# Optimization experiments

Measured on AMD Instinct MI355X. Metric: run time of the kernel, lower is better.

The kernel has to match this reference:

```python
import jax, jax.numpy as jnp
import numpy as np

N = 100000
F = 512
D = 128
E = 1600000

def setup_inputs() -> dict:
    key = jax.random.key(0)
    k1, k2, k3, k4, k5 = jax.random.split(key, 5)
    feature = jax.random.normal(k1, (N, F), dtype=jnp.float32)
    W = jax.random.normal(k2, (F, D), dtype=jnp.float32) * (1.0 / np.sqrt(D))
    bias = jax.random.normal(k3, (D,), dtype=jnp.float32) * (1.0 / np.sqrt(D))
    edge_vals = jax.random.uniform(k4, (E,), dtype=jnp.float32)
    edge_index = jax.random.randint(k5, (2, E), 0, N, dtype=jnp.int32)
    return {"feature": feature, "W": W, "bias": bias,
            "edge_vals": edge_vals, "edge_index": edge_index}

def reference(feature, W, bias, edge_vals, edge_index):
    # support = relu(feature @ W)                          [N, D]
    support = jax.nn.relu(feature @ W)
    row, col = edge_index[0], edge_index[1]
    # spmm(adj, support): gather source rows, scale, scatter-add to dest rows
    msgs = edge_vals[:, None] * support[col]               # [E, D]
    agg = jax.ops.segment_sum(msgs, row, num_segments=feature.shape[0])
    # adj_low = adj + I  ->  identity contributes +support; then + bias
    return agg + support + bias
```

## Files before the change

### kernel.cpp

```cpp
#include <hip/hip_runtime.h>
#include <hip/hip_bf16.h>

typedef __attribute__((ext_vector_type(8))) __bf16 bf16x8;
typedef __attribute__((ext_vector_type(4))) float f32x4;

#define F_DIM 512
#define D_DIM 128
#define RPB 128
#define MAXBUK 1024
#define BIN_CHUNK 8192

__device__ __forceinline__ unsigned short f32_to_bf16_rn(float x) {
    union { float f; unsigned u; } v; v.f = x;
    unsigned u = v.u;
    unsigned rounded = u + 0x7fffu + ((u >> 16) & 1u);
    return (unsigned short)(rounded >> 16);
}
__device__ __forceinline__ float bf16_to_f32(unsigned short u) {
    return __uint_as_float((unsigned)u << 16);
}

__global__ void wt_kernel(const float* __restrict__ W, unsigned short* __restrict__ Wt) {
    int idx = blockIdx.x * blockDim.x + threadIdx.x;
    int n = idx >> 9;
    int k = idx & 511;
    Wt[idx] = f32_to_bf16_rn(W[k * D_DIM + n]);
}

__global__ __launch_bounds__(256) void gemm_relu_pipe(
    const float* __restrict__ A,
    const unsigned short* __restrict__ Bt,
    unsigned short* __restrict__ Sb,
    int Nrows)
{
    __shared__ unsigned short Al[2 * 64 * 40];
    __shared__ unsigned short Bl[2 * 128 * 40];

    const int tid  = threadIdx.x;
    const int wave = tid >> 6;
    const int lane = tid & 63;
    const int g    = lane >> 4;
    const int r16  = lane & 15;
    const int m0   = blockIdx.x * 64;

    const int sar = tid >> 2;
    const int skq = tid & 3;
    int arow = m0 + sar;
    if (arow >= Nrows) arow = Nrows - 1;
    const float* aptr = A + (size_t)arow * F_DIM + skq * 8;
    const int awoff = sar * 40 + skq * 8;

    const int sbr = tid >> 1;
    const int skh = tid & 1;
    const unsigned short* bptr = Bt + (size_t)sbr * F_DIM + skh * 16;
    const int bwoff = sbr * 40 + skh * 16;

    float4 ar0, ar1;
    uint4  br0, br1;

    auto loadAB = [&](int ks) {
        const float4* pa = (const float4*)(aptr + ks * 32);
        ar0 = pa[0]; ar1 = pa[1];
        const uint4* pb = (const uint4*)(bptr + ks * 32);
        br0 = pb[0]; br1 = pb[1];
    };
    auto storeAB = [&](int buf) {
        union { uint4 q; __bf16 h[8]; } u;
        u.h[0]=(__bf16)ar0.x; u.h[1]=(__bf16)ar0.y; u.h[2]=(__bf16)ar0.z; u.h[3]=(__bf16)ar0.w;
        u.h[4]=(__bf16)ar1.x; u.h[5]=(__bf16)ar1.y; u.h[6]=(__bf16)ar1.z; u.h[7]=(__bf16)ar1.w;
        *(uint4*)&Al[buf * 2560 + awoff] = u.q;
        unsigned short* bw = &Bl[buf * 5120 + bwoff];
        *(uint4*)bw       = br0;
        *(uint4*)(bw + 8) = br1;
    };

    f32x4 acc[8];
#pragma unroll
    for (int j = 0; j < 8; ++j) acc[j] = (f32x4)0.0f;

    loadAB(0);
    storeAB(0);
    __syncthreads();

#pragma unroll
    for (int ks = 0; ks < 16; ++ks) {
        const int cur = ks & 1;
        if (ks < 15) loadAB(ks + 1);

        const unsigned short* Ab = Al + cur * 2560;
        const unsigned short* Bb = Bl + cur * 5120;
        bf16x8 af = *(const bf16x8*)&Ab[(wave * 16 + r16) * 40 + g * 8];
#pragma unroll
        for (int nf = 0; nf < 8; ++nf) {
            bf16x8 bf = *(const bf16x8*)&Bb[(nf * 16 + r16) * 40 + g * 8];
            acc[nf] = __builtin_amdgcn_mfma_f32_16x16x32_bf16(af, bf, acc[nf], 0, 0, 0);
        }

        if (ks < 15) storeAB(cur ^ 1);
        __syncthreads();
    }

#pragma unroll
    for (int nf = 0; nf < 8; ++nf) {
#pragma unroll
        for (int r = 0; r < 4; ++r) {
            int row = m0 + wave * 16 + g * 4 + r;
            if (row < Nrows) {
                float v = acc[nf][r];
                Sb[(size_t)row * D_DIM + nf * 16 + r16] = f32_to_bf16_rn(v > 0.f ? v : 0.f);
            }
        }
    }
}

__global__ void cursor_init_kernel(int* __restrict__ cursor, int nbuk, int cap) {
    int i = blockIdx.x * blockDim.x + threadIdx.x;
    if (i < nbuk) cursor[i] = i * cap;
}

__global__ __launch_bounds__(256) void bin_kernel(
    const int* __restrict__ ei, const float* __restrict__ ev,
    int* __restrict__ cursor, uint2* __restrict__ ecv, int E, int nbuk)
{
    __shared__ int cnt[MAXBUK];
    __shared__ int bas[MAXBUK];
    const int tid = threadIdx.x;
    const int e0 = blockIdx.x * BIN_CHUNK;
    const int e1 = min(e0 + BIN_CHUNK, E);

    for (int i = tid; i < nbuk; i += 256) cnt[i] = 0;
    __syncthreads();
    for (int e = e0 + tid; e < e1; e += 256)
        atomicAdd(&cnt[ei[e] >> 7], 1);
    __syncthreads();
    for (int i = tid; i < nbuk; i += 256) {
        int c = cnt[i];
        bas[i] = c ? atomicAdd(&cursor[i], c) : 0;
        cnt[i] = 0;
    }
    __syncthreads();
    for (int e = e0 + tid; e < e1; e += 256) {
        int r = ei[e];
        int b = r >> 7;
        int slot = atomicAdd(&cnt[b], 1);
        uint2 cv;
        cv.x = ((unsigned)ei[E + e] << 7) | (unsigned)(r & 127);
        cv.y = __float_as_uint(ev[e]);
        ecv[(size_t)bas[b] + slot] = cv;
    }
}

__global__ __launch_bounds__(256) void bsort_kernel(
    const uint2* __restrict__ ecv, const int* __restrict__ cursor,
    uint2* __restrict__ ecv2, int* __restrict__ rowoff, int* __restrict__ rowcnt,
    int cap, int Nrows)
{
    __shared__ int cnt[RPB];
    __shared__ int base[RPB];
    const int tid = threadIdx.x;
    const int b   = blockIdx.x;
    const int beg = b * cap;
    const int end = cursor[b];

    if (tid < RPB) cnt[tid] = 0;
    __syncthreads();
    for (int i = beg + tid; i < end; i += 256)
        atomicAdd(&cnt[ecv[i].x & 127], 1);
    __syncthreads();
    if (tid < 64) {
        int carry = 0;
#pragma unroll
        for (int c = 0; c < 2; ++c) {
            int idx = c * 64 + tid;
            int v = cnt[idx];
            int orig = v;
            for (int d = 1; d < 64; d <<= 1) {
                int t = __shfl_up(v, d, 64);
                if (tid >= d) v += t;
            }
            base[idx] = carry + v - orig;
            carry += __shfl(v, 63, 64);
        }
    }
    __syncthreads();
    if (tid < RPB) {
        int r = b * RPB + tid;
        if (r < Nrows) {
            rowoff[r] = beg + base[tid];
            rowcnt[r] = cnt[tid];
        }
        cnt[tid] = 0;
    }
    __syncthreads();
    for (int i = beg + tid; i < end; i += 256) {
        uint2 cv = ecv[i];
        int rl = cv.x & 127;
        int slot = atomicAdd(&cnt[rl], 1);
        ecv2[(size_t)beg + base[rl] + slot] = cv;
    }
}

__global__ __launch_bounds__(256) void accum_kernel(
    const uint2* __restrict__ ecv2, const int* __restrict__ rowoff,
    const int* __restrict__ rowcnt, const unsigned short* __restrict__ Sb,
    const float* __restrict__ bias, float* __restrict__ out, int n)
{
    int wid = (blockIdx.x * 256 + threadIdx.x) >> 6;
    if (wid >= n) return;
    int lane = threadIdx.x & 63;
    int c2 = lane * 2;

    int start = rowoff[wid];
    int end   = start + rowcnt[wid];

    float ax = 0.f, ay = 0.f;
    int i = start;
    for (; i + 3 < end; i += 4) {
        uint2 cv0 = ecv2[i];
        uint2 cv1 = ecv2[i + 1];
        uint2 cv2 = ecv2[i + 2];
        uint2 cv3 = ecv2[i + 3];
        ushort2 s0 = *(const ushort2*)&Sb[(size_t)(cv0.x >> 7) * D_DIM + c2];
        ushort2 s1 = *(const ushort2*)&Sb[(size_t)(cv1.x >> 7) * D_DIM + c2];
        ushort2 s2 = *(const ushort2*)&Sb[(size_t)(cv2.x >> 7) * D_DIM + c2];
        ushort2 s3 = *(const ushort2*)&Sb[(size_t)(cv3.x >> 7) * D_DIM + c2];
        float v0 = __uint_as_float(cv0.y);
        float v1 = __uint_as_float(cv1.y);
        float v2 = __uint_as_float(cv2.y);
        float v3 = __uint_as_float(cv3.y);
        ax += v0 * bf16_to_f32(s0.x) + v1 * bf16_to_f32(s1.x)
            + v2 * bf16_to_f32(s2.x) + v3 * bf16_to_f32(s3.x);
        ay += v0 * bf16_to_f32(s0.y) + v1 * bf16_to_f32(s1.y)
            + v2 * bf16_to_f32(s2.y) + v3 * bf16_to_f32(s3.y);
    }
    for (; i < end; ++i) {
        uint2 cv = ecv2[i];
        ushort2 s = *(const ushort2*)&Sb[(size_t)(cv.x >> 7) * D_DIM + c2];
        float v = __uint_as_float(cv.y);
        ax += v * bf16_to_f32(s.x);
        ay += v * bf16_to_f32(s.y);
    }

    ushort2 so = *(const ushort2*)&Sb[(size_t)wid * D_DIM + c2];
    float2 b = *(const float2*)&bias[c2];
    float2 o;
    o.x = ax + bf16_to_f32(so.x) + b.x;
    o.y = ay + bf16_to_f32(so.y) + b.y;
    *(float2*)&out[(size_t)wid * D_DIM + c2] = o;
}

extern "C" void kernel_launch(void* const* d_in, const int* in_sizes, int n_in,
                              void* d_out, int out_size, void* d_ws, size_t ws_size,
                              hipStream_t stream) {
    const float* feature = (const float*)d_in[0];
    const float* W       = (const float*)d_in[1];
    const float* bias    = (const float*)d_in[2];
    const float* ev      = (const float*)d_in[3];
    const int*   ei      = (const int*)d_in[4];
    float* out = (float*)d_out;

    const int N = in_sizes[0] / F_DIM;
    const int E = in_sizes[3];
    const int nbuk = (N + RPB - 1) / RPB;
    int cap = (E + nbuk - 1) / nbuk;
    cap = cap + cap / 4 + 256;

    char* ws = (char*)d_ws;
    size_t cur = 0;
    auto alloc = [&](size_t bytes) -> void* {
        void* p = ws + cur;
        cur = (cur + bytes + 255) & ~(size_t)255;
        return p;
    };
    unsigned short* Sb     = (unsigned short*)alloc((size_t)N * D_DIM * 2);
    unsigned short* Wt     = (unsigned short*)alloc((size_t)D_DIM * F_DIM * 2);
    int*            cursor = (int*)alloc((size_t)nbuk * 4);
    int*            rowoff = (int*)alloc((size_t)N * 4);
    int*            rowcnt = (int*)alloc((size_t)N * 4);
    uint2*          ecv    = (uint2*)alloc(((size_t)nbuk * cap + BIN_CHUNK) * 8);
    uint2*          ecv2   = (uint2*)alloc(((size_t)nbuk * cap + BIN_CHUNK) * 8);
    (void)ws_size;

    wt_kernel<<<(F_DIM * D_DIM) / 256, 256, 0, stream>>>(W, Wt);
    gemm_relu_pipe<<<(N + 63) / 64, 256, 0, stream>>>(feature, Wt, Sb, N);
    cursor_init_kernel<<<(nbuk + 255) / 256, 256, 0, stream>>>(cursor, nbuk, cap);
    bin_kernel<<<(E + BIN_CHUNK - 1) / BIN_CHUNK, 256, 0, stream>>>(ei, ev, cursor, ecv, E, nbuk);
    bsort_kernel<<<nbuk, 256, 0, stream>>>(ecv, cursor, ecv2, rowoff, rowcnt, cap, N);
    accum_kernel<<<(N + 3) / 4, 256, 0, stream>>>(ecv2, rowoff, rowcnt, Sb, bias, out, N);
}
```

Before: 220.1 us.

## Fuse bucket sort with row accumulation in shared memory, merge prep kernels

Bucket sorting and row aggregation now run in one kernel. Each 512-thread block loads its bucket's edges into shared memory, counting-sorts them by local row there, and then accumulates its 128 rows directly. This drops the ecv2, rowoff and rowcnt global round trips and one launch. W transposition and cursor initialisation are folded into a single prep kernel. Per-bucket capacity is clamped to 3072 entries to fit shared memory (48 KB of edge buffers). That is safe for these uniform inputs but could overflow on skewed degree distributions. Each block now covers 128 rows with 8 waves, which lowers parallelism in the gather phase.

```diff
diff --git a/kernel.cpp b/kernel.cpp
--- a/kernel.cpp
+++ b/kernel.cpp
@@ -9,6 +9,7 @@
 #define RPB 128
 #define MAXBUK 1024
 #define BIN_CHUNK 8192
+#define CAPMAX 3072
 
 __device__ __forceinline__ unsigned short f32_to_bf16_rn(float x) {
     union { float f; unsigned u; } v; v.f = x;
@@ -20,11 +21,17 @@
     return __uint_as_float((unsigned)u << 16);
 }
 
-__global__ void wt_kernel(const float* __restrict__ W, unsigned short* __restrict__ Wt) {
-    int idx = blockIdx.x * blockDim.x + threadIdx.x;
-    int n = idx >> 9;
-    int k = idx & 511;
-    Wt[idx] = f32_to_bf16_rn(W[k * D_DIM + n]);
+__global__ void prep_kernel(const float* __restrict__ W, unsigned short* __restrict__ Wt,
+                            int* __restrict__ cursor, int nbuk, int cap) {
+    int b = blockIdx.x;
+    if (b < 256) {
+        int idx = b * 256 + threadIdx.x;
+        int n = idx >> 9;
+        int k = idx & 511;
+        Wt[idx] = f32_to_bf16_rn(W[k * D_DIM + n]);
+    } else {
+        for (int i = threadIdx.x; i < nbuk; i += 256) cursor[i] = i * cap;
+    }
 }
 
 __global__ __launch_bounds__(256) void gemm_relu_pipe(
@@ -113,11 +120,6 @@
     }
 }
 
-__global__ void cursor_init_kernel(int* __restrict__ cursor, int nbuk, int cap) {
-    int i = blockIdx.x * blockDim.x + threadIdx.x;
-    if (i < nbuk) cursor[i] = i * cap;
-}
-
 __global__ __launch_bounds__(256) void bin_kernel(
     const int* __restrict__ ei, const float* __restrict__ ev,
     int* __restrict__ cursor, uint2* __restrict__ ecv, int E, int nbuk)
@@ -150,22 +152,29 @@
     }
 }
 
-__global__ __launch_bounds__(256) void bsort_kernel(
+__global__ __launch_bounds__(512) void sortaccum_kernel(
     const uint2* __restrict__ ecv, const int* __restrict__ cursor,
-    uint2* __restrict__ ecv2, int* __restrict__ rowoff, int* __restrict__ rowcnt,
-    int cap, int Nrows)
+    const unsigned short* __restrict__ Sb, const float* __restrict__ bias,
+    float* __restrict__ out, int Nrows, int cap)
 {
+    __shared__ uint2 raw[CAPMAX];
+    __shared__ uint2 srt[CAPMAX];
     __shared__ int cnt[RPB];
     __shared__ int base[RPB];
+    __shared__ int scur[RPB];
+
     const int tid = threadIdx.x;
     const int b   = blockIdx.x;
     const int beg = b * cap;
-    const int end = cursor[b];
+    const int n   = cursor[b] - beg;
 
     if (tid < RPB) cnt[tid] = 0;
     __syncthreads();
-    for (int i = beg + tid; i < end; i += 256)
-        atomicAdd(&cnt[ecv[i].x & 127], 1);
+    for (int i = tid; i < n; i += 512) {
+        uint2 cv = ecv[beg + i];
+        raw[i] = cv;
+        atomicAdd(&cnt[cv.x & 127], 1);
+    }
     __syncthreads();
     if (tid < 64) {
         int carry = 0;
@@ -178,75 +187,67 @@
                 int t = __shfl_up(v, d, 64);
                 if (tid >= d) v += t;
             }
-            base[idx] = carry + v - orig;
+            int excl = carry + v - orig;
+            base[idx] = excl;
+            scur[idx] = excl;
             carry += __shfl(v, 63, 64);
         }
     }
     __syncthreads();
-    if (tid < RPB) {
-        int r = b * RPB + tid;
-        if (r < Nrows) {
-            rowoff[r] = beg + base[tid];
-            rowcnt[r] = cnt[tid];
-        }
-        cnt[tid] = 0;
-    }
-    __syncthreads();
-    for (int i = beg + tid; i < end; i += 256) {
-        uint2 cv = ecv[i];
-        int rl = cv.x & 127;
-        int slot = atomicAdd(&cnt[rl], 1);
-        ecv2[(size_t)beg + base[rl] + slot] = cv;
-    }
-}
-
-__global__ __launch_bounds__(256) void accum_kernel(
-    const uint2* __restrict__ ecv2, const int* __restrict__ rowoff,
-    const int* __restrict__ rowcnt, const unsigned short* __restrict__ Sb,
-    const float* __restrict__ bias, float* __restrict__ out, int n)
-{
-    int wid = (blockIdx.x * 256 + threadIdx.x) >> 6;
-    if (wid >= n) return;
-    int lane = threadIdx.x & 63;
-    int c2 = lane * 2;
-
-    int start = rowoff[wid];
-    int end   = start + rowcnt[wid];
-
-    float ax = 0.f, ay = 0.f;
-    int i = start;
-    for (; i + 3 < end; i += 4) {
-        uint2 cv0 = ecv2[i];
-        uint2 cv1 = ecv2[i + 1];
-        uint2 cv2 = ecv2[i + 2];
-        uint2 cv3 = ecv2[i + 3];
-        ushort2 s0 = *(const ushort2*)&Sb[(size_t)(cv0.x >> 7) * D_DIM + c2];
-        ushort2 s1 = *(const ushort2*)&Sb[(size_t)(cv1.x >> 7) * D_DIM + c2];
-        ushort2 s2 = *(const ushort2*)&Sb[(size_t)(cv2.x >> 7) * D_DIM + c2];
-        ushort2 s3 = *(const ushort2*)&Sb[(size_t)(cv3.x >> 7) * D_DIM + c2];
-        float v0 = __uint_as_float(cv0.y);
-        float v1 = __uint_as_float(cv1.y);
-        float v2 = __uint_as_float(cv2.y);
-        float v3 = __uint_as_float(cv3.y);
-        ax += v0 * bf16_to_f32(s0.x) + v1 * bf16_to_f32(s1.x)
-            + v2 * bf16_to_f32(s2.x) + v3 * bf16_to_f32(s3.x);
-        ay += v0 * bf16_to_f32(s0.y) + v1 * bf16_to_f32(s1.y)
-            + v2 * bf16_to_f32(s2.y) + v3 * bf16_to_f32(s3.y);
-    }
-    for (; i < end; ++i) {
-        uint2 cv = ecv2[i];
-        ushort2 s = *(const ushort2*)&Sb[(size_t)(cv.x >> 7) * D_DIM + c2];
-        float v = __uint_as_float(cv.y);
-        ax += v * bf16_to_f32(s.x);
-        ay += v * bf16_to_f32(s.y);
-    }
-
-    ushort2 so = *(const ushort2*)&Sb[(size_t)wid * D_DIM + c2];
-    float2 b = *(const float2*)&bias[c2];
-    float2 o;
-    o.x = ax + bf16_to_f32(so.x) + b.x;
-    o.y = ay + bf16_to_f32(so.y) + b.y;
-    *(float2*)&out[(size_t)wid * D_DIM + c2] = o;
+    for (int i = tid; i < n; i += 512) {
+        uint2 cv = raw[i];
+        int slot = atomicAdd(&scur[cv.x & 127], 1);
+        srt[slot] = cv;
+    }
+    __syncthreads();
+
+    const int wv   = tid >> 6;
+    const int lane = tid & 63;
+    const int c2   = lane * 2;
+    const int r0g  = b * RPB;
+
+    for (int rr = 0; rr < 16; ++rr) {
+        int rl  = wv * 16 + rr;
+        int row = r0g + rl;
+        if (row >= Nrows) break;
+        int s = base[rl];
+        int e = s + cnt[rl];
+
+        float ax = 0.f, ay = 0.f;
+        int i = s;
+        for (; i + 3 < e; i += 4) {
+            uint2 cv0 = srt[i];
+            uint2 cv1 = srt[i + 1];
+            uint2 cv2 = srt[i + 2];
+            uint2 cv3 = srt[i + 3];
+            ushort2 s0 = *(const ushort2*)&Sb[(size_t)(cv0.x >> 7) * D_DIM + c2];
+            ushort2 s1 = *(const ushort2*)&Sb[(size_t)(cv1.x >> 7) * D_DIM + c2];
+            ushort2 s2 = *(const ushort2*)&Sb[(size_t)(cv2.x >> 7) * D_DIM + c2];
+            ushort2 s3 = *(const ushort2*)&Sb[(size_t)(cv3.x >> 7) * D_DIM + c2];
+            float v0 = __uint_as_float(cv0.y);
+            float v1 = __uint_as_float(cv1.y);
+            float v2 = __uint_as_float(cv2.y);
+            float v3 = __uint_as_float(cv3.y);
+            ax += v0 * bf16_to_f32(s0.x) + v1 * bf16_to_f32(s1.x)
+                + v2 * bf16_to_f32(s2.x) + v3 * bf16_to_f32(s3.x);
+            ay += v0 * bf16_to_f32(s0.y) + v1 * bf16_to_f32(s1.y)
+                + v2 * bf16_to_f32(s2.y) + v3 * bf16_to_f32(s3.y);
+        }
+        for (; i < e; ++i) {
+            uint2 cv = srt[i];
+            ushort2 sv = *(const ushort2*)&Sb[(size_t)(cv.x >> 7) * D_DIM + c2];
+            float v = __uint_as_float(cv.y);
+            ax += v * bf16_to_f32(sv.x);
+            ay += v * bf16_to_f32(sv.y);
+        }
+
+        ushort2 so = *(const ushort2*)&Sb[(size_t)row * D_DIM + c2];
+        float2 bv = *(const float2*)&bias[c2];
+        float2 o;
+        o.x = ax + bf16_to_f32(so.x) + bv.x;
+        o.y = ay + bf16_to_f32(so.y) + bv.y;
+        *(float2*)&out[(size_t)row * D_DIM + c2] = o;
+    }
 }
 
 extern "C" void kernel_launch(void* const* d_in, const int* in_sizes, int n_in,
@@ -264,6 +265,7 @@
     const int nbuk = (N + RPB - 1) / RPB;
     int cap = (E + nbuk - 1) / nbuk;
     cap = cap + cap / 4 + 256;
+    if (cap > CAPMAX) cap = CAPMAX;
 
     char* ws = (char*)d_ws;
     size_t cur = 0;
@@ -275,16 +277,11 @@
     unsigned short* Sb     = (unsigned short*)alloc((size_t)N * D_DIM * 2);
     unsigned short* Wt     = (unsigned short*)alloc((size_t)D_DIM * F_DIM * 2);
     int*            cursor = (int*)alloc((size_t)nbuk * 4);
-    int*            rowoff = (int*)alloc((size_t)N * 4);
-    int*            rowcnt = (int*)alloc((size_t)N * 4);
     uint2*          ecv    = (uint2*)alloc(((size_t)nbuk * cap + BIN_CHUNK) * 8);
-    uint2*          ecv2   = (uint2*)alloc(((size_t)nbuk * cap + BIN_CHUNK) * 8);
     (void)ws_size;
 
-    wt_kernel<<<(F_DIM * D_DIM) / 256, 256, 0, stream>>>(W, Wt);
+    prep_kernel<<<257, 256, 0, stream>>>(W, Wt, cursor, nbuk, cap);
     gemm_relu_pipe<<<(N + 63) / 64, 256, 0, stream>>>(feature, Wt, Sb, N);
-    cursor_init_kernel<<<(nbuk + 255) / 256, 256, 0, stream>>>(cursor, nbuk, cap);
     bin_kernel<<<(E + BIN_CHUNK - 1) / BIN_CHUNK, 256, 0, stream>>>(ei, ev, cursor, ecv, E, nbuk);
-    bsort_kernel<<<nbuk, 256, 0, stream>>>(ecv, cursor, ecv2, rowoff, rowcnt, cap, N);
-    accum_kernel<<<(N + 3) / 4, 256, 0, stream>>>(ecv2, rowoff, rowcnt, Sb, bias, out, N);
-}
+    sortaccum_kernel<<<nbuk, 512, 0, stream>>>(ecv, cursor, Sb, bias, out, N, cap);
+}
```

New measurement: 224.7 us. +2.1%, slower.
